# Optimization experiments

Measured on AMD Instinct MI355X. Metric: run time of the kernel, lower is better.

The kernel has to match this reference:

```python
import jax, jax.numpy as jnp
import numpy as np

N_STRUCT = 16384
N_ATOMS = 2048
VOCAB = 100


def setup_inputs() -> dict:
    key = jax.random.key(0)
    k_idx, k_val = jax.random.split(key)
    index = jax.random.randint(k_idx, (N_STRUCT, N_ATOMS), 0, VOCAB, dtype=jnp.int64 if jax.config.jax_enable_x64 else jnp.int32)
    values = jax.random.normal(k_val, (VOCAB,), dtype=jnp.float32)
    return {"index": index, "values": values}


def reference(index, values):
    # batch_compute: output[s, a] = values[index[s, a]]
    # Original loops over vocab with masked_fill; equivalent math is a gather.
    return jnp.take(values, index, axis=0)  # [n_structure, n_atoms]
```

## Files before the change

### kernel.cpp

```cpp
#include <hip/hip_runtime.h>


constexpr int VOCAB = 100;

typedef int   vint4   __attribute__((ext_vector_type(4)));
typedef float vfloat4 __attribute__((ext_vector_type(4)));

__global__ __launch_bounds__(1024) void gather_kernel(
    const vint4* __restrict__ idx4,
    const float* __restrict__ vals,
    vfloat4* __restrict__ out4)
{
    __shared__ float svals[VOCAB];
    if (threadIdx.x < VOCAB) svals[threadIdx.x] = vals[threadIdx.x];
    __syncthreads();

    const int t = blockIdx.x * blockDim.x + threadIdx.x;

    vint4 v = __builtin_nontemporal_load(&idx4[t]);
    vfloat4 o = { svals[v.x], svals[v.y], svals[v.z], svals[v.w] };
    __builtin_nontemporal_store(o, &out4[t]);
}

extern "C" void kernel_launch(void* const* d_in, const int* in_sizes, int n_in,
                              void* d_out, int out_size, void* d_ws, size_t ws_size,
                              hipStream_t stream) {
    const int*   idx  = (const int*)d_in[0];
    const float* vals = (const float*)d_in[1];
    float*       out  = (float*)d_out;

    int n  = in_sizes[0];
    int n4 = n / 4;

    const int block = 1024;
    const int grid  = n4 / block;

    gather_kernel<<<grid, block, 0, stream>>>(
        (const vint4*)idx, vals, (vfloat4*)out);
}
```

Before: 218.2 us.

## Use per-wave LDS table copies, drop block barrier, process four vectors per thread

Each wavefront now loads the value table into its own private LDS slice and waits only on its own LDS writes with s_waitcnt instead of a block-wide __syncthreads. Each thread handles four int4 index vectors, issuing all global loads up front to keep more memory requests in flight, and the grid shrinks by four. This removes the block barrier and spreads the table setup over more work per block. The trade-offs are more LDS per block and reliance on wavefront-synchronous execution for correctness.

```diff
diff --git a/kernel.cpp b/kernel.cpp
--- a/kernel.cpp
+++ b/kernel.cpp
@@ -11,15 +11,34 @@
     const float* __restrict__ vals,
     vfloat4* __restrict__ out4)
 {
-    __shared__ float svals[VOCAB];
-    if (threadIdx.x < VOCAB) svals[threadIdx.x] = vals[threadIdx.x];
-    __syncthreads();
+    __shared__ float svals[16 * 128];
 
-    const int t = blockIdx.x * blockDim.x + threadIdx.x;
+    const int lane = threadIdx.x & 63;
+    const int wid  = threadIdx.x >> 6;
+    float* wt = &svals[wid * 128];
 
-    vint4 v = __builtin_nontemporal_load(&idx4[t]);
-    vfloat4 o = { svals[v.x], svals[v.y], svals[v.z], svals[v.w] };
-    __builtin_nontemporal_store(o, &out4[t]);
+    float v_lo = vals[lane];
+    float v_hi = (lane < VOCAB - 64) ? vals[64 + lane] : 0.f;
+
+    const int t = blockIdx.x * 4096 + threadIdx.x;
+
+    vint4 v0 = __builtin_nontemporal_load(&idx4[t]);
+    vint4 v1 = __builtin_nontemporal_load(&idx4[t + 1024]);
+    vint4 v2 = __builtin_nontemporal_load(&idx4[t + 2048]);
+    vint4 v3 = __builtin_nontemporal_load(&idx4[t + 3072]);
+
+    wt[lane] = v_lo;
+    if (lane < VOCAB - 64) wt[64 + lane] = v_hi;
+    asm volatile("s_waitcnt lgkmcnt(0)" ::: "memory");
+
+    vfloat4 o0 = { wt[v0.x], wt[v0.y], wt[v0.z], wt[v0.w] };
+    __builtin_nontemporal_store(o0, &out4[t]);
+    vfloat4 o1 = { wt[v1.x], wt[v1.y], wt[v1.z], wt[v1.w] };
+    __builtin_nontemporal_store(o1, &out4[t + 1024]);
+    vfloat4 o2 = { wt[v2.x], wt[v2.y], wt[v2.z], wt[v2.w] };
+    __builtin_nontemporal_store(o2, &out4[t + 2048]);
+    vfloat4 o3 = { wt[v3.x], wt[v3.y], wt[v3.z], wt[v3.w] };
+    __builtin_nontemporal_store(o3, &out4[t + 3072]);
 }
 
 extern "C" void kernel_launch(void* const* d_in, const int* in_sizes, int n_in,
@@ -33,7 +52,8 @@
     int n4 = n / 4;
 
     const int block = 1024;
-    const int grid  = n4 / block;
+    const int per_block = block * 4;
+    const int grid  = n4 / per_block;
 
     gather_kernel<<<grid, block, 0, stream>>>(
         (const vint4*)idx, vals, (vfloat4*)out);
```

Measured after the change: 219.7 us. About the same (+0.7%).
